# Kernel tuning notes

Hardware: AMD Instinct MI355X
Metric: run time of the kernel (lower is better)

Reference implementation:

```python
import jax, jax.numpy as jnp
import numpy as np


def setup_inputs() -> dict:
    key = jax.random.key(0)
    kx, kd = jax.random.split(key)
    B, C, T_phone = 32, 512, 1024
    x = jax.random.normal(kx, (B, C, T_phone), dtype=jnp.float32)
    durations = jax.random.randint(kd, (B, T_phone), 0, 8, dtype=jnp.int32)
    return {"x": x, "durations": durations}


def reference(x, durations):
    # x: [B, C, T_phone] float; durations: [B, T_phone] int
    B, C, T_phone = x.shape
    cum = jnp.cumsum(durations, axis=1)            # [B, T_phone] exclusive-end frame offsets
    total = cum[:, -1]                             # [B] total frames per utterance
    max_frames = int(jnp.max(total))               # T_frame (data-dependent, computed eagerly)
    t = jnp.arange(max_frames)                     # [T_frame]
    # frame t belongs to the first phone p with cum[b, p] > t (zero-duration phones skipped)
    p = jax.vmap(lambda c: jnp.searchsorted(c, t, side="right"))(cum)  # [B, T_frame]
    valid = t[None, :] < total[:, None]            # [B, T_frame] frames inside utterance
    p = jnp.clip(p, 0, T_phone - 1)
    idx = jnp.broadcast_to(p[:, None, :], (B, C, max_frames))
    out = jnp.take_along_axis(x, idx, axis=2)      # [B, C, T_frame] gather phone features
    out = jnp.where(valid[:, None, :], out, jnp.zeros((), dtype=x.dtype))
    mel_mask = ~valid                              # True where padding (matches torch ref)
    return out, mel_mask
```

## Files before the change

### kernel.cpp

```cpp
#include <hip/hip_runtime.h>

#define B 32
#define C 512
#define TP 1024
#define CHUNK 32

__global__ void __launch_bounds__(256) cumsum_k(const int* __restrict__ dur,
                                                int* __restrict__ cum) {
    const int b = blockIdx.x, tid = threadIdx.x;
    const int lane = tid & 63, wid = tid >> 6;
    int4 v = ((const int4*)(dur + b * TP))[tid];
    const int s1 = v.x + v.y, s2 = s1 + v.z, s3 = s2 + v.w;
    int val = s3;
    #pragma unroll
    for (int off = 1; off < 64; off <<= 1) {
        int n = __shfl_up(val, off, 64);
        if (lane >= off) val += n;
    }
    __shared__ int wtot[4];
    if (lane == 63) wtot[wid] = val;
    __syncthreads();
    int base = 0;
    #pragma unroll
    for (int w = 0; w < 4; ++w)
        if (w < wid) base += wtot[w];
    const int excl = base + val - s3;
    int4 o;
    o.x = excl + v.x; o.y = excl + s1; o.z = excl + s2; o.w = excl + s3;
    ((int4*)(cum + b * TP))[tid] = o;
}

__global__ void __launch_bounds__(256) phone_k(const int* __restrict__ cum,
                                               int* __restrict__ pidx,
                                               float* __restrict__ mask,
                                               int MF) {
    __shared__ int scum[TP];
    const int b = blockIdx.y;
    for (int i = threadIdx.x; i < TP; i += 256) scum[i] = cum[b * TP + i];
    __syncthreads();
    const int t = blockIdx.x * 256 + threadIdx.x;
    if (t >= MF) return;
    const int total = scum[TP - 1];
    int lo = 0, hi = TP;
    while (lo < hi) {
        int mid = (lo + hi) >> 1;
        if (scum[mid] <= t) lo = mid + 1; else hi = mid;
    }
    const bool valid = (t < total);
    pidx[(size_t)b * MF + t] = valid ? (lo < TP - 1 ? lo : TP - 1) : -1;
    mask[(size_t)b * MF + t] = valid ? 0.0f : 1.0f;
}

__global__ void __launch_bounds__(256) gather_k(const float* __restrict__ x,
                                                const int* __restrict__ pidx,
                                                float* __restrict__ out,
                                                int MF) {
    const int b = blockIdx.y, z = blockIdx.z;
    const int tbase = blockIdx.x * 1024 + threadIdx.x;
    const int* pb = pidx + (size_t)b * MF;

    int t[4], p[4], q[4];
    #pragma unroll
    for (int j = 0; j < 4; ++j) {
        t[j] = tbase + j * 256;
        p[j] = (t[j] < MF) ? pb[t[j]] : -2;
        q[j] = p[j] >= 0 ? p[j] : 0;
    }

    const float* xb = x   + ((size_t)b * C + (size_t)z * CHUNK) * TP;
    float*       ob = out + ((size_t)b * C + (size_t)z * CHUNK) * MF;

    #pragma unroll 2
    for (int c = 0; c < CHUNK; ++c) {
        const float* xr = xb + (size_t)c * TP;
        float* orow     = ob + (size_t)c * MF;
        #pragma unroll
        for (int j = 0; j < 4; ++j) {
            if (p[j] != -2) {
                float v = xr[q[j]];
                orow[t[j]] = (p[j] >= 0) ? v : 0.0f;
            }
        }
    }
}

extern "C" void kernel_launch(void* const* d_in, const int* in_sizes, int n_in,
                              void* d_out, int out_size, void* d_ws, size_t ws_size,
                              hipStream_t stream) {
    const float* x   = (const float*)d_in[0];
    const int*   dur = (const int*)d_in[1];
    float* out = (float*)d_out;

    const int MF = out_size / (B * (C + 1));
    float* mask = out + (size_t)B * C * MF;

    int* cum  = (int*)d_ws;
    int* pidx = cum + (size_t)B * TP;

    cumsum_k<<<B, 256, 0, stream>>>(dur, cum);

    dim3 pgrid((MF + 255) / 256, B);
    phone_k<<<pgrid, 256, 0, stream>>>(cum, pidx, mask, MF);

    dim3 ggrid((MF + 1023) / 1024, B, C / CHUNK);
    gather_k<<<ggrid, 256, 0, stream>>>(x, pidx, out, MF);
}
```

Baseline: 374.4 us.

## Fuse phone-index search into gather kernel and vectorize output stores

Removes the separate phone_k kernel and its pidx workspace. Each gather block now loads the cumsum into shared memory, binary-searches once per thread for four consecutive frames, walks forward to find the remaining indices, and the z==0 blocks write the mask. Output rows are written as float4 when MF is a multiple of 4. This saves a kernel launch and the pidx global round trip, and makes stores wider. In exchange the search is recomputed in every channel-chunk block.

```diff
diff --git a/kernel.cpp b/kernel.cpp
--- a/kernel.cpp
+++ b/kernel.cpp
@@ -30,41 +30,50 @@
     ((int4*)(cum + b * TP))[tid] = o;
 }
 
-__global__ void __launch_bounds__(256) phone_k(const int* __restrict__ cum,
-                                               int* __restrict__ pidx,
-                                               float* __restrict__ mask,
-                                               int MF) {
+template <bool VEC>
+__global__ void __launch_bounds__(256) gather_k(const float* __restrict__ x,
+                                                const int* __restrict__ cum,
+                                                float* __restrict__ out,
+                                                float* __restrict__ mask,
+                                                int MF) {
     __shared__ int scum[TP];
-    const int b = blockIdx.y;
-    for (int i = threadIdx.x; i < TP; i += 256) scum[i] = cum[b * TP + i];
+    const int b = blockIdx.y, z = blockIdx.z;
+    ((int4*)scum)[threadIdx.x] = ((const int4*)(cum + b * TP))[threadIdx.x];
     __syncthreads();
-    const int t = blockIdx.x * 256 + threadIdx.x;
-    if (t >= MF) return;
+
+    const int t0 = blockIdx.x * 1024 + threadIdx.x * 4;
+    if (t0 >= MF) return;
     const int total = scum[TP - 1];
+
     int lo = 0, hi = TP;
     while (lo < hi) {
         int mid = (lo + hi) >> 1;
-        if (scum[mid] <= t) lo = mid + 1; else hi = mid;
+        if (scum[mid] <= t0) lo = mid + 1; else hi = mid;
     }
-    const bool valid = (t < total);
-    pidx[(size_t)b * MF + t] = valid ? (lo < TP - 1 ? lo : TP - 1) : -1;
-    mask[(size_t)b * MF + t] = valid ? 0.0f : 1.0f;
-}
-
-__global__ void __launch_bounds__(256) gather_k(const float* __restrict__ x,
-                                                const int* __restrict__ pidx,
-                                                float* __restrict__ out,
-                                                int MF) {
-    const int b = blockIdx.y, z = blockIdx.z;
-    const int tbase = blockIdx.x * 1024 + threadIdx.x;
-    const int* pb = pidx + (size_t)b * MF;
-
-    int t[4], p[4], q[4];
+    int q[4]; bool val[4];
+    int pc = lo;
     #pragma unroll
     for (int j = 0; j < 4; ++j) {
-        t[j] = tbase + j * 256;
-        p[j] = (t[j] < MF) ? pb[t[j]] : -2;
-        q[j] = p[j] >= 0 ? p[j] : 0;
+        const int tj = t0 + j;
+        while (pc < TP && scum[pc] <= tj) ++pc;
+        q[j] = pc < TP - 1 ? pc : TP - 1;
+        val[j] = (tj < total) && (tj < MF);
+    }
+
+    const bool full = VEC && (t0 + 4 <= MF);
+
+    if (z == 0) {
+        float m[4];
+        #pragma unroll
+        for (int j = 0; j < 4; ++j) m[j] = (t0 + j < total) ? 0.0f : 1.0f;
+        float* mrow = mask + (size_t)b * MF + t0;
+        if (full) {
+            *(float4*)mrow = make_float4(m[0], m[1], m[2], m[3]);
+        } else {
+            #pragma unroll
+            for (int j = 0; j < 4; ++j)
+                if (t0 + j < MF) mrow[j] = m[j];
+        }
     }
 
     const float* xb = x   + ((size_t)b * C + (size_t)z * CHUNK) * TP;
@@ -73,13 +82,20 @@
     #pragma unroll 2
     for (int c = 0; c < CHUNK; ++c) {
         const float* xr = xb + (size_t)c * TP;
-        float* orow     = ob + (size_t)c * MF;
-        #pragma unroll
-        for (int j = 0; j < 4; ++j) {
-            if (p[j] != -2) {
-                float v = xr[q[j]];
-                orow[t[j]] = (p[j] >= 0) ? v : 0.0f;
-            }
+        float l0 = xr[q[0]], l1 = xr[q[1]], l2 = xr[q[2]], l3 = xr[q[3]];
+        float4 v;
+        v.x = val[0] ? l0 : 0.0f;
+        v.y = val[1] ? l1 : 0.0f;
+        v.z = val[2] ? l2 : 0.0f;
+        v.w = val[3] ? l3 : 0.0f;
+        float* orow = ob + (size_t)c * MF + t0;
+        if (full) {
+            *(float4*)orow = v;
+        } else {
+            const float vv[4] = {v.x, v.y, v.z, v.w};
+            #pragma unroll
+            for (int j = 0; j < 4; ++j)
+                if (t0 + j < MF) orow[j] = vv[j];
         }
     }
 }
@@ -94,14 +110,13 @@
     const int MF = out_size / (B * (C + 1));
     float* mask = out + (size_t)B * C * MF;
 
-    int* cum  = (int*)d_ws;
-    int* pidx = cum + (size_t)B * TP;
+    int* cum = (int*)d_ws;
 
     cumsum_k<<<B, 256, 0, stream>>>(dur, cum);
 
-    dim3 pgrid((MF + 255) / 256, B);
-    phone_k<<<pgrid, 256, 0, stream>>>(cum, pidx, mask, MF);
-
     dim3 ggrid((MF + 1023) / 1024, B, C / CHUNK);
-    gather_k<<<ggrid, 256, 0, stream>>>(x, pidx, out, MF);
+    if ((MF & 3) == 0)
+        gather_k<true><<<ggrid, 256, 0, stream>>>(x, cum, out, mask, MF);
+    else
+        gather_k<false><<<ggrid, 256, 0, stream>>>(x, cum, out, mask, MF);
 }
```

After: 359.1 us. 4.1% less time.
